# Kernel optimization log

Hardware: AMD Instinct MI355X
Metric: run time of the kernel (lower is better)

Reference implementation:

```python
import jax, jax.numpy as jnp
import numpy as np

SR = 16000
FLEN = 400        # round(winlen * samplerate)
STEP = 160        # round(winstep * samplerate)
NFFT = 512
NFILT = 26
NUMCEP = 13
PREEMPH = 0.97
CEPLIFTER = 22
LOWFREQ = 0.0
HIGHFREQ = SR / 2.0
EPS = float(np.finfo(np.float32).eps)


def _hz2mel(hz):
    return 2595.0 * np.log10(1.0 + hz / 700.0)


def _mel2hz(mel):
    return 700.0 * (10.0 ** (mel / 2595.0) - 1.0)


def _filterbanks():
    # [NFFT//2+1, NFILT] mel triangular filterbank (transposed, as used in torch.mm)
    melpoints = np.linspace(_hz2mel(LOWFREQ), _hz2mel(HIGHFREQ), NFILT + 2)
    bins = np.floor((NFFT + 1) * _mel2hz(melpoints) / SR)
    fb = np.zeros([NFILT, NFFT // 2 + 1], dtype=np.float64)
    for j in range(NFILT):
        for i in range(int(bins[j]), int(bins[j + 1])):
            fb[j, i] = (i - bins[j]) / (bins[j + 1] - bins[j])
        for i in range(int(bins[j + 1]), int(bins[j + 2])):
            fb[j, i] = (bins[j + 2] - i) / (bins[j + 2] - bins[j + 1])
    return fb.T  # [257, 26]


def _dct_mat(N, k):
    # orthonormal DCT-II matrix rows 0..k-1: [k, N]
    n = np.arange(N)
    kk = np.arange(k)[:, None]
    C = np.cos(np.pi * (2 * n[None, :] + 1) * kk / (2.0 * N))
    C[0] *= 1.0 / np.sqrt(N)
    C[1:] *= np.sqrt(2.0 / N)
    return C


def setup_inputs() -> dict:
    key = jax.random.key(0)
    k1, k2 = jax.random.split(key)
    signals = jax.random.normal(k1, (64, 320000), dtype=jnp.float32)
    lengths = jax.random.randint(k2, (64,), 0, 320000, dtype=jnp.int32)
    return {"signals": signals, "lengths": lengths}


def reference(signals, lengths):
    B, T = signals.shape
    F = 1 if T <= FLEN else 1 + int(np.ceil((T - FLEN) / float(STEP)))
    padlen = (F - 1) * STEP + FLEN

    # preemphasis (uses self.preemph=0.97), masked past each sample's length
    pre = jnp.concatenate(
        [signals[:, :1], signals[:, 1:] - PREEMPH * signals[:, :-1]], axis=1)
    pos = jnp.arange(T)
    pre = jnp.where(pos[None, :] < lengths[:, None], pre, jnp.zeros((), pre.dtype))

    # framing: [B, F, FLEN]
    pad = jnp.pad(pre, ((0, 0), (0, padlen - T)))
    idx = np.arange(FLEN)[None, :] + STEP * np.arange(F)[:, None]
    frames = pad[:, idx]

    # power spectrum, [B, F, NFFT//2+1]
    spec = jnp.fft.rfft(frames, n=NFFT, axis=-1)
    pspec = (spec.real * spec.real + spec.imag * spec.imag) / NFFT
    energy = pspec.sum(-1) + EPS                      # [B, F]

    fb = jnp.asarray(_filterbanks(), dtype=signals.dtype)     # [257, 26]
    feat = jnp.log(pspec @ fb + EPS)                  # [B, F, 26]

    dctm = jnp.asarray(_dct_mat(NFILT, NUMCEP), dtype=signals.dtype)  # [13, 26]
    ceps = jnp.einsum('bfn,kn->bfk', feat, dctm)      # [B, F, 13]

    n = jnp.arange(NUMCEP, dtype=signals.dtype)
    lift = 1.0 + (CEPLIFTER / 2.0) * jnp.sin(np.pi * n / CEPLIFTER)
    ceps = ceps * lift
    ceps = ceps.at[:, :, 0].set(jnp.log(energy))       # appendEnergy

    # per-sample number of frames; zero-pad rest (original pads to batch max)
    nframes = jnp.where(
        lengths <= FLEN, 1,
        1 + jnp.ceil((lengths - FLEN) / float(STEP)).astype(jnp.int32))
    fmask = jnp.arange(F)[None, :] < nframes[:, None]
    ceps = jnp.where(fmask[:, :, None], ceps, jnp.zeros((), ceps.dtype))
    return ceps, nframes
```

## Files before the change

### kernel.cpp

```cpp
#include <hip/hip_runtime.h>
#include <math.h>

#define SRATE   16000
#define FLEN    400
#define STEP    160
#define NFFT    512
#define NBINS   257
#define NFILT   26
#define NUMCEP  13
#define BATCH   64
#define TLEN    320000
#define NFRAMES 1999
#define EPSF    1.1920929e-07f
#define PI_F    3.14159265358979323846f

#define CEPS_N  (BATCH * NFRAMES * NUMCEP)

typedef float    v2f __attribute__((ext_vector_type(2)));
typedef unsigned uv2 __attribute__((ext_vector_type(2)));

__device__ __forceinline__ v2f mk2(float a, float b) { v2f v; v.x = a; v.y = b; return v; }
__device__ __forceinline__ v2f pfma(v2f a, v2f b, v2f c) { return __builtin_elementwise_fma(a, b, c); }

template<int CTRL>
__device__ __forceinline__ float fdpp(float x) {
    return __builtin_bit_cast(float, __builtin_amdgcn_mov_dpp(
        __builtin_bit_cast(int, x), CTRL, 0xF, 0xF, true));
}
template<int IMM>
__device__ __forceinline__ float fswz(float x) {
    return __builtin_bit_cast(float, __builtin_amdgcn_ds_swizzle(
        __builtin_bit_cast(int, x), IMM));
}
__device__ __forceinline__ uv2 pl32(float x) {
    unsigned u = __builtin_bit_cast(unsigned, x);
    return __builtin_amdgcn_permlane32_swap(u, u, false, false);
}
__device__ __forceinline__ float fxor32(float x, bool hi32) {
    uv2 r = pl32(x);
    return __builtin_bit_cast(float, hi32 ? r[0] : r[1]);
}
#if __has_builtin(__builtin_amdgcn_permlane16_swap)
__device__ __forceinline__ float fxor16(float x, bool hi16) {
    unsigned u = __builtin_bit_cast(unsigned, x);
    uv2 r = __builtin_amdgcn_permlane16_swap(u, u, false, false);
    return __builtin_bit_cast(float, hi16 ? r[0] : r[1]);
}
#define SH_X16(v) fxor16(v, hi_)
#else
#define SH_X16(v) fswz<0x401F>(v)
#endif

#define DPP_X1   0xB1
#define DPP_X2   0x4E
#define DPP_X8   0x128
#define SWZ_X4   0x101F
#define SWZ_X16  0x401F

#define WS_DCT  32
#define WS_QOFF 370

__global__ void mfcc_setup_kernel(const int* __restrict__ lengths,
                                  void* __restrict__ ws,
                                  float* __restrict__ out_nframes) {
    int tid = threadIdx.x;
    int*   bins = (int*)ws;
    float* dctw = (float*)ws + WS_DCT;
    int*   qoff = (int*)ws + WS_QOFF;

    if (tid < 28) {
        double M    = 2595.0 * log10(1.0 + 8000.0 / 700.0);
        double step = M / 27.0;
        double mel  = (tid == 27) ? M : (double)tid * step;
        double hz   = 700.0 * (pow(10.0, mel / 2595.0) - 1.0);
        bins[tid] = (int)floor((double)(NFFT + 1) * hz / (double)SRATE);
    }
    for (int t = tid; t < NUMCEP * NFILT; t += 64) {
        int k = t / NFILT, j = t - k * NFILT;
        double v = cos(M_PI * (double)((2 * j + 1) * k) / (2.0 * (double)NFILT));
        v *= (k == 0) ? 1.0 / sqrt((double)NFILT) : sqrt(2.0 / (double)NFILT);
        double lift = 1.0 + 11.0 * sin(M_PI * (double)k / 22.0);
        dctw[t] = (float)(v * lift);
    }
    {
        int len = lengths[tid];
        int nf  = (len <= FLEN) ? 1 : 1 + (len - FLEN + STEP - 1) / STEP;
        out_nframes[tid] = (float)nf;
        int x = (nf + 3) >> 2;
        #pragma unroll
        for (int off = 1; off < 64; off <<= 1) {
            int y = __shfl_up(x, off);
            if (tid >= off) x += y;
        }
        qoff[tid + 1] = x;
        if (tid == 0) qoff[0] = 0;
    }
}

__global__ void mfcc_zero_kernel(float4* __restrict__ p) {
    int i = blockIdx.x * blockDim.x + threadIdx.x;
    if (i < CEPS_N / 4) p[i] = float4{0.0f, 0.0f, 0.0f, 0.0f};
}

__launch_bounds__(256, 2)
__global__ void mfcc_kernel(const float* __restrict__ sig,
                            const int*   __restrict__ lengths,
                            const void*  __restrict__ ws,
                            float*       __restrict__ out) {
    __shared__ v2f psA[4][260];
    __shared__ v2f psB[4][260];
    __shared__ v2f featAs[4][28], featBs[4][28];
    __shared__ float dctS[NUMCEP * NFILT];
    __shared__ int   binsS[NFILT + 2];

    const int tid  = threadIdx.x;
    const int lane = tid & 63;
    const int w    = tid >> 6;

    const int* qoffG = (const int*)ws + WS_QOFF;
    const int total = qoffG[64];
    if ((int)blockIdx.x * 4 >= total) return;

    {
        const int*   binsG = (const int*)ws;
        const float* dctG  = (const float*)ws + WS_DCT;
        for (int t = tid; t < NUMCEP * NFILT; t += 256) dctS[t] = dctG[t];
        if (tid < NFILT + 2) binsS[tid] = binsG[tid];
    }
    __syncthreads();

    const int L = blockIdx.x * 4 + w;
    if (L >= total) return;
    int qv = qoffG[lane];
    unsigned long long mm = __ballot(qv <= L);
    const int b  = __popcll(mm) - 1;
    const int q  = L - qoffG[b];
    const int f0 = 4 * q;
    const int len = lengths[b];
    const int nf  = (len <= FLEN) ? 1 : 1 + (len - FLEN + STEP - 1) / STEP;

    const float* s = sig + (long)b * TLEN;
    const int base = f0 * STEP;

    const int B   = (int)(__brev((unsigned)lane) >> 26);
    const int i0  = 8 * B;
    const bool liveB = (i0 < FLEN);

    v2f Zr0[4], Zi0[4], Zr1[4], Zi1[4];
    const bool fastw = (base >= 1) && (base + 880 <= len);
    if (fastw) {
        float w0[9], w1[9], w2[9], w3[9];
        if (liveB) {
            const float4* sv = (const float4*)(s + base + i0);
            float4 a0 = sv[-1],  a1 = sv[0],   a2 = sv[1];
            float4 b0 = sv[39],  b1 = sv[40],  b2 = sv[41];
            float4 c0 = sv[79],  c1 = sv[80],  c2 = sv[81];
            float4 d0 = sv[119], d1 = sv[120], d2 = sv[121];
#define UNPK(W, q0, q1, q2)                                                   \
            W[0] = q0.w; W[1] = q1.x; W[2] = q1.y; W[3] = q1.z; W[4] = q1.w;  \
            W[5] = q2.x; W[6] = q2.y; W[7] = q2.z; W[8] = q2.w;
            UNPK(w0, a0, a1, a2)
            UNPK(w1, b0, b1, b2)
            UNPK(w2, c0, c1, c2)
            UNPK(w3, d0, d1, d2)
#undef UNPK
        } else {
            #pragma unroll
            for (int j = 0; j < 9; ++j) { w0[j] = w1[j] = w2[j] = w3[j] = 0.0f; }
        }
        #pragma unroll
        for (int m = 0; m < 4; ++m) {
            const int j = (m == 0) ? 0 : (m == 1) ? 4 : (m == 2) ? 2 : 6;
            Zr0[m] = mk2(fmaf(-0.97f, w0[j],     w0[j + 1]),
                         fmaf(-0.97f, w0[j + 1], w0[j + 2]));
            Zi0[m] = mk2(fmaf(-0.97f, w1[j],     w1[j + 1]),
                         fmaf(-0.97f, w1[j + 1], w1[j + 2]));
            Zr1[m] = mk2(fmaf(-0.97f, w2[j],     w2[j + 1]),
                         fmaf(-0.97f, w2[j + 1], w2[j + 2]));
            Zi1[m] = mk2(fmaf(-0.97f, w3[j],     w3[j + 1]),
                         fmaf(-0.97f, w3[j + 1], w3[j + 2]));
        }
    } else {
        float w0[9], w1[9], w2[9], w3[9];
        const int tb0 = base + i0 - 1;
        #pragma unroll
        for (int j = 0; j < 9; ++j) {
            int t0 = tb0 + j;
            w0[j] = (liveB && t0 >= 0 && t0 < len) ? s[t0] : 0.0f;
            int t1 = t0 + 160; w1[j] = (liveB && t1 < len) ? s[t1] : 0.0f;
            int t2 = t0 + 320; w2[j] = (liveB && t2 < len) ? s[t2] : 0.0f;
            int t3 = t0 + 480; w3[j] = (liveB && t3 < len) ? s[t3] : 0.0f;
        }
        const int tbe = base + i0;
        #pragma unroll
        for (int m = 0; m < 4; ++m) {
            const int j = (m == 0) ? 0 : (m == 1) ? 4 : (m == 2) ? 2 : 6;
#define ASMW(Wk, OFF, DST)                                                    \
            { float va = fmaf(-0.97f, Wk[j],     Wk[j + 1]);                  \
              float vb = fmaf(-0.97f, Wk[j + 1], Wk[j + 2]);                  \
              bool ma = liveB && (tbe + (OFF) + j)     < len;                 \
              bool mb = liveB && (tbe + (OFF) + j + 1) < len;                 \
              DST = mk2(ma ? va : 0.0f, mb ? vb : 0.0f); }
            ASMW(w0, 0,   Zr0[m])
            ASMW(w1, 160, Zi0[m])
            ASMW(w2, 320, Zr1[m])
            ASMW(w3, 480, Zi1[m])
#undef ASMW
        }
    }

    const float ang = -PI_F * (float)lane / 256.0f;
    float T1i = __sinf(ang);
    float T1r = __cosf(ang);
#define SQC(orr, oii, ir, ii) { float _r = ir * ir - ii * ii; oii = 2.0f * ir * ii; orr = _r; }
    float T2r, T2i;   SQC(T2r, T2i, T1r, T1i)
    float T4r, T4i;   SQC(T4r, T4i, T2r, T2i)
    float T8r, T8i;   SQC(T8r, T8i, T4r, T4i)
    float T16r, T16i; SQC(T16r, T16i, T8r, T8i)
    float T32r, T32i; SQC(T32r, T32i, T16r, T16i)
    float T64r, T64i; SQC(T64r, T64i, T32r, T32i)
    float T128r, T128i; SQC(T128r, T128i, T64r, T64i)
    const float RH = 0.70710678118654752f;
    const float A1r = RH * (T1r + T1i), A1i = RH * (T1i - T1r);
    const float A2r = T1i,              A2i = -T1r;
    const float A3r = RH * (T1i - T1r), A3i = -RH * (T1r + T1i);

    {
        const float sg = (lane & 1) ? -1.0f : 1.0f;
        const v2f sg2 = mk2(sg, sg);
        #pragma unroll
        for (int m = 0; m < 4; ++m) {
            v2f pr0 = mk2(fdpp<DPP_X1>(Zr0[m].x), fdpp<DPP_X1>(Zr0[m].y));
            v2f pi0 = mk2(fdpp<DPP_X1>(Zi0[m].x), fdpp<DPP_X1>(Zi0[m].y));
            v2f pr1 = mk2(fdpp<DPP_X1>(Zr1[m].x), fdpp<DPP_X1>(Zr1[m].y));
            v2f pi1 = mk2(fdpp<DPP_X1>(Zi1[m].x), fdpp<DPP_X1>(Zi1[m].y));
            Zr0[m] = pfma(sg2, Zr0[m], pr0);
            Zi0[m] = pfma(sg2, Zi0[m], pi0);
            Zr1[m] = pfma(sg2, Zr1[m], pr1);
            Zi1[m] = pfma(sg2, Zi1[m], pi1);
        }
    }

#define PK_XSTAGE2(d, UR, UI, SH)                                             \
    {                                                                         \
        const bool hi_ = (lane & (d)) != 0;                                   \
        const float ur = hi_ ? (UR) : 1.0f;                                   \
        const float ui = hi_ ? (UI) : 0.0f;                                   \
        const float sg = hi_ ? 1.0f : -1.0f;                                  \
        const v2f ur2 = mk2(ur, ur), ui2 = mk2(ui, ui);                       \
        const v2f nui2 = mk2(-ui, -ui), sg2 = mk2(sg, sg);                    \
        _Pragma("unroll")                                                     \
        for (int m = 0; m < 4; ++m) {                                         \
            v2f tr0 = pfma(Zi0[m], nui2, Zr0[m] * ur2);                       \
            v2f ti0 = pfma(Zi0[m], ur2,  Zr0[m] * ui2);                       \
            v2f tr1 = pfma(Zi1[m], nui2, Zr1[m] * ur2);                       \
            v2f ti1 = pfma(Zi1[m], ur2,  Zr1[m] * ui2);                       \
            v2f pr0 = mk2(SH(tr0.x), SH(tr0.y));                              \
            v2f pi0 = mk2(SH(ti0.x), SH(ti0.y));                              \
            v2f pr1 = mk2(SH(tr1.x), SH(tr1.y));                              \
            v2f pi1 = mk2(SH(ti1.x), SH(ti1.y));                              \
            Zr0[m] = pfma(sg2, pr0, tr0);                                     \
            Zi0[m] = pfma(sg2, pi0, ti0);                                     \
            Zr1[m] = pfma(sg2, pr1, tr1);                                     \
            Zi1[m] = pfma(sg2, pi1, ti1);                                     \
        }                                                                     \
    }
#define SH_X2(v)  fdpp<DPP_X2>(v)
#define SH_X4(v)  fswz<SWZ_X4>(v)
#define SH_X8(v)  fdpp<DPP_X8>(v)
#define SH_X32(v) fxor32(v, hi_)
    PK_XSTAGE2(2,  T128r, T128i, SH_X2)
    PK_XSTAGE2(4,  T64r,  T64i,  SH_X4)
    PK_XSTAGE2(8,  T32r,  T32i,  SH_X8)
    PK_XSTAGE2(16, T16r,  T16i,  SH_X16)
    PK_XSTAGE2(32, T8r,   T8i,   SH_X32)

#define PBFLY2(A, Bv, WR, WI)                                                 \
    {                                                                         \
        const v2f wr2 = mk2((WR), (WR)), wi2 = mk2((WI), (WI));               \
        const v2f nwi2 = mk2(-(WI), -(WI));                                   \
        v2f tr0 = pfma(Zi0[Bv], nwi2, Zr0[Bv] * wr2);                         \
        v2f ti0 = pfma(Zi0[Bv], wr2,  Zr0[Bv] * wi2);                         \
        v2f tr1 = pfma(Zi1[Bv], nwi2, Zr1[Bv] * wr2);                         \
        v2f ti1 = pfma(Zi1[Bv], wr2,  Zr1[Bv] * wi2);                         \
        Zr0[Bv] = Zr0[A] - tr0;  Zi0[Bv] = Zi0[A] - ti0;                      \
        Zr0[A]  = Zr0[A] + tr0;  Zi0[A]  = Zi0[A] + ti0;                      \
        Zr1[Bv] = Zr1[A] - tr1;  Zi1[Bv] = Zi1[A] - ti1;                      \
        Zr1[A]  = Zr1[A] + tr1;  Zi1[A]  = Zi1[A] + ti1;                      \
    }
    PBFLY2(0, 1, T4r, T4i)
    PBFLY2(2, 3, T4r, T4i)
    PBFLY2(0, 2, T2r, T2i)
    PBFLY2(1, 3, T2i, -T2r)

    float zrA[8], ziA[8], zrB[8], ziB[8];
    #pragma unroll
    for (int m = 0; m < 4; ++m) {
        const float Wr = (m == 0) ? T1r : (m == 1) ? A1r : (m == 2) ? A2r : A3r;
        const float Wi = (m == 0) ? T1i : (m == 1) ? A1i : (m == 2) ? A2i : A3i;
        { float tr = Zr0[m].y * Wr - Zi0[m].y * Wi;
          float ti = Zr0[m].y * Wi + Zi0[m].y * Wr;
          zrA[m]     = Zr0[m].x + tr;  ziA[m]     = Zi0[m].x + ti;
          zrA[m + 4] = Zr0[m].x - tr;  ziA[m + 4] = Zi0[m].x - ti; }
        { float tr = Zr1[m].y * Wr - Zi1[m].y * Wi;
          float ti = Zr1[m].y * Wi + Zi1[m].y * Wr;
          zrB[m]     = Zr1[m].x + tr;  ziB[m]     = Zi1[m].x + ti;
          zrB[m + 4] = Zr1[m].x - tr;  ziB[m + 4] = Zi1[m].x - ti; }
    }

    v2f* PA = psA[w];
    v2f* PB = psB[w];
    const float inv = 1.0f / (4.0f * (float)NFFT);
    v2f eA = mk2(0.0f, 0.0f), eB = mk2(0.0f, 0.0f);
    const int ml = (64 - lane) & 63;
    #pragma unroll
    for (int r = 0; r < 4; ++r) {
        float mrA = __shfl(zrA[7 - r], ml), miA = __shfl(ziA[7 - r], ml);
        float mrB = __shfl(zrB[7 - r], ml), miB = __shfl(ziB[7 - r], ml);
        if (lane == 0) {
            mrA = zrA[(8 - r) & 7]; miA = ziA[(8 - r) & 7];
            mrB = zrB[(8 - r) & 7]; miB = ziB[(8 - r) & 7];
        }
        { float ar = zrA[r] + mrA, ai = ziA[r] - miA;
          float br = ziA[r] + miA, bi = zrA[r] - mrA;
          v2f p = mk2((ar * ar + ai * ai) * inv, (br * br + bi * bi) * inv);
          PA[64 * r + lane] = p;  eA += p; }
        { float ar = zrB[r] + mrB, ai = ziB[r] - miB;
          float br = ziB[r] + miB, bi = zrB[r] - mrB;
          v2f p = mk2((ar * ar + ai * ai) * inv, (br * br + bi * bi) * inv);
          PB[64 * r + lane] = p;  eB += p; }
    }
    if (lane == 0) {
        v2f pA = mk2(4.0f * zrA[4] * zrA[4] * inv, 4.0f * ziA[4] * ziA[4] * inv);
        v2f pB = mk2(4.0f * zrB[4] * zrB[4] * inv, 4.0f * ziB[4] * ziB[4] * inv);
        PA[256] = pA;  eA += pA;
        PB[256] = pB;  eB += pB;
    }
#define ERED(E)                                                               \
    E = E + mk2(fdpp<DPP_X1>(E.x),  fdpp<DPP_X1>(E.y));                       \
    E = E + mk2(fdpp<DPP_X2>(E.x),  fdpp<DPP_X2>(E.y));                       \
    E = E + mk2(fswz<SWZ_X4>(E.x),  fswz<SWZ_X4>(E.y));                       \
    E = E + mk2(fdpp<DPP_X8>(E.x),  fdpp<DPP_X8>(E.y));                       \
    E = E + mk2(fswz<SWZ_X16>(E.x), fswz<SWZ_X16>(E.y));                      \
    { uv2 rx = pl32(E.x), ry = pl32(E.y);                                     \
      E = mk2(__builtin_bit_cast(float, rx[0]) + __builtin_bit_cast(float, rx[1]), \
              __builtin_bit_cast(float, ry[0]) + __builtin_bit_cast(float, ry[1])); }
    ERED(eA)
    ERED(eB)
    __builtin_amdgcn_wave_barrier();

    const int  j  = lane & 31;
    const bool hi = lane >= 32;
    {
        const v2f* P = hi ? PB : PA;
        v2f fu = mk2(0, 0), fs = mk2(0, 0), fu2 = mk2(0, 0), fs2 = mk2(0, 0);
        if (j <= NFILT) {
            int bA = binsS[j], bZ = binsS[j + 1];
            int i = bA;
            for (; i + 1 < bZ; i += 2) {
                v2f p = P[i], p2 = P[i + 1];
                float c0 = (float)(i - bA), c1 = (float)(i + 1 - bA);
                fs  += p;   fu  = pfma(p,  mk2(c0, c0), fu);
                fs2 += p2;  fu2 = pfma(p2, mk2(c1, c1), fu2);
            }
            if (i < bZ) {
                v2f p = P[i];
                float c0 = (float)(i - bA);
                fs += p;  fu = pfma(p, mk2(c0, c0), fu);
            }
            fs += fs2;  fu += fu2;
            float iw = (bZ > bA) ? 1.0f / (float)(bZ - bA) : 0.0f;
            fu = fu * mk2(iw, iw);
        }
        v2f down = fs - fu;
        v2f dn = mk2(__shfl(down.x, lane + 1), __shfl(down.y, lane + 1));
        if (j < NFILT) {
            v2f ft = fu + dn;
            v2f fv = mk2(__logf(ft.x + EPSF), __logf(ft.y + EPSF));
            if (hi) featBs[w][j] = fv; else featAs[w][j] = fv;
        }
    }
    __builtin_amdgcn_wave_barrier();

    if (j < NUMCEP) {
        const v2f* ft = hi ? featBs[w] : featAs[w];
        v2f a0 = mk2(0, 0), a1 = mk2(0, 0);
        #pragma unroll
        for (int jj = 0; jj < NFILT; jj += 2) {
            float c0 = dctS[j * NFILT + jj], c1 = dctS[j * NFILT + jj + 1];
            a0 = pfma(ft[jj],     mk2(c0, c0), a0);
            a1 = pfma(ft[jj + 1], mk2(c1, c1), a1);
        }
        v2f val = a0 + a1;
        if (j == 0) {
            v2f E = hi ? eB : eA;
            val = mk2(__logf(E.x + EPSF), __logf(E.y + EPSF));
        }
        const int fb = f0 + (hi ? 2 : 0);
        long o0 = ((long)b * NFRAMES + fb) * NUMCEP + j;
        if (fb < nf)     out[o0]          = val.x;
        if (fb + 1 < nf) out[o0 + NUMCEP] = val.y;
    }
}

extern "C" void kernel_launch(void* const* d_in, const int* in_sizes, int n_in,
                              void* d_out, int out_size, void* d_ws, size_t ws_size,
                              hipStream_t stream) {
    const float* sig     = (const float*)d_in[0];
    const int*   lengths = (const int*)d_in[1];
    float* out = (float*)d_out;

    mfcc_zero_kernel<<<(CEPS_N / 4 + 255) / 256, 256, 0, stream>>>((float4*)out);
    mfcc_setup_kernel<<<1, 64, 0, stream>>>(lengths, d_ws, out + (size_t)CEPS_N);

    mfcc_kernel<<<8000, 256, 0, stream>>>(sig, lengths, d_ws, out);
}
```

Before: 54.99 us.

## Fold output zeroing into idle blocks of main kernel, zeroing only dead frames

Removes the separate kernel that zeroed the whole ceps output. The setup kernel now also builds a prefix sum of dead frame counts per sample. Blocks of the main MFCC kernel that have no frames to compute instead zero only the frames past each sample's length, finding the sample with a binary search. The launch-bounds attribute also changes to waves_per_eu(2,4). This saves a kernel launch and the redundant writes to frames that are overwritten anyway, but adds a divide and a binary search per zeroed element and scalar stores that are not coalesced.

```diff
diff --git a/kernel.cpp b/kernel.cpp
--- a/kernel.cpp
+++ b/kernel.cpp
@@ -14,7 +14,7 @@
 #define EPSF    1.1920929e-07f
 #define PI_F    3.14159265358979323846f
 
-#define CEPS_N  (BATCH * NFRAMES * NUMCEP)
+#define GRID_MAIN 8000
 
 typedef float    v2f __attribute__((ext_vector_type(2)));
 typedef unsigned uv2 __attribute__((ext_vector_type(2)));
@@ -59,6 +59,7 @@
 
 #define WS_DCT  32
 #define WS_QOFF 370
+#define WS_DOFF 440
 
 __global__ void mfcc_setup_kernel(const int* __restrict__ lengths,
                                   void* __restrict__ ws,
@@ -67,6 +68,7 @@
     int*   bins = (int*)ws;
     float* dctw = (float*)ws + WS_DCT;
     int*   qoff = (int*)ws + WS_QOFF;
+    int*   doff = (int*)ws + WS_DOFF;
 
     if (tid < 28) {
         double M    = 2595.0 * log10(1.0 + 8000.0 / 700.0);
@@ -87,26 +89,24 @@
         int nf  = (len <= FLEN) ? 1 : 1 + (len - FLEN + STEP - 1) / STEP;
         out_nframes[tid] = (float)nf;
         int x = (nf + 3) >> 2;
+        int d = NFRAMES - nf;
         #pragma unroll
         for (int off = 1; off < 64; off <<= 1) {
-            int y = __shfl_up(x, off);
-            if (tid >= off) x += y;
+            int y  = __shfl_up(x, off);
+            int y2 = __shfl_up(d, off);
+            if (tid >= off) { x += y; d += y2; }
         }
         qoff[tid + 1] = x;
-        if (tid == 0) qoff[0] = 0;
-    }
-}
-
-__global__ void mfcc_zero_kernel(float4* __restrict__ p) {
-    int i = blockIdx.x * blockDim.x + threadIdx.x;
-    if (i < CEPS_N / 4) p[i] = float4{0.0f, 0.0f, 0.0f, 0.0f};
-}
-
-__launch_bounds__(256, 2)
-__global__ void mfcc_kernel(const float* __restrict__ sig,
-                            const int*   __restrict__ lengths,
-                            const void*  __restrict__ ws,
-                            float*       __restrict__ out) {
+        doff[tid + 1] = d;
+        if (tid == 0) { qoff[0] = 0; doff[0] = 0; }
+    }
+}
+
+__global__ __launch_bounds__(256) __attribute__((amdgpu_waves_per_eu(2, 4)))
+void mfcc_kernel(const float* __restrict__ sig,
+                 const int*   __restrict__ lengths,
+                 const void*  __restrict__ ws,
+                 float*       __restrict__ out) {
     __shared__ v2f psA[4][260];
     __shared__ v2f psB[4][260];
     __shared__ v2f featAs[4][28], featBs[4][28];
@@ -119,7 +119,29 @@
 
     const int* qoffG = (const int*)ws + WS_QOFF;
     const int total = qoffG[64];
-    if ((int)blockIdx.x * 4 >= total) return;
+
+    if ((int)blockIdx.x * 4 >= total) {
+        const int* doffG = (const int*)ws + WS_DOFF;
+        const int liveBlocks = (total + 3) >> 2;
+        const int deadFrames = doffG[64];
+        const long deadFloats = (long)deadFrames * NUMCEP;
+        const long stride = (long)(GRID_MAIN - liveBlocks) * 256;
+        for (long idx = (long)(blockIdx.x - liveBlocks) * 256 + tid;
+             idx < deadFloats; idx += stride) {
+            int F = (int)(idx / 13);
+            int k = (int)(idx - 13L * F);
+            int lo = 0, hi = 64;
+            #pragma unroll
+            for (int it = 0; it < 6; ++it) {
+                int mid = (lo + hi) >> 1;
+                if (doffG[mid] <= F) lo = mid; else hi = mid;
+            }
+            int nf2 = NFRAMES - (doffG[lo + 1] - doffG[lo]);
+            int f   = nf2 + (F - doffG[lo]);
+            out[((long)lo * NFRAMES + f) * NUMCEP + k] = 0.0f;
+        }
+        return;
+    }
 
     {
         const int*   binsG = (const int*)ws;
@@ -410,8 +432,8 @@
     const int*   lengths = (const int*)d_in[1];
     float* out = (float*)d_out;
 
-    mfcc_zero_kernel<<<(CEPS_N / 4 + 255) / 256, 256, 0, stream>>>((float4*)out);
-    mfcc_setup_kernel<<<1, 64, 0, stream>>>(lengths, d_ws, out + (size_t)CEPS_N);
-
-    mfcc_kernel<<<8000, 256, 0, stream>>>(sig, lengths, d_ws, out);
-}
+    mfcc_setup_kernel<<<1, 64, 0, stream>>>(lengths, d_ws,
+                                            out + (size_t)BATCH * NFRAMES * NUMCEP);
+
+    mfcc_kernel<<<GRID_MAIN, 256, 0, stream>>>(sig, lengths, d_ws, out);
+}
```

Measured after the change: 50.58 us. -8.0%, faster.
